# Kernel tuning notes

Measured on AMD Instinct MI355X. Metric: run time of the kernel, lower is better.

The kernel has to match this reference:

```python
import jax, jax.numpy as jnp
import numpy as np

B, S, D_IN, D, H, HD, HALF, L = 64, 500, 64, 128, 8, 16, 5, 2
WIN = 2 * HALF + 1  # 11 attended positions per query
EPS = 1e-12  # HF layer_norm_eps default


def _ln(x, g, b):
    m = x.mean(-1, keepdims=True)
    v = ((x - m) ** 2).mean(-1, keepdims=True)
    return (x - m) / jnp.sqrt(v + EPS) * g + b


def setup_inputs() -> dict:
    key = jax.random.key(0)
    ks = jax.random.split(key, 24)
    n = lambda i, shape: jax.random.normal(ks[i], shape, jnp.float32) * 0.02
    return {
        "x": jax.random.normal(ks[0], (B, S, D_IN), jnp.float32),
        "W_in": n(1, (D_IN, D)), "b_in": jnp.zeros((D,), jnp.float32),
        "pos_emb": n(2, (512, D)), "tt_emb": n(3, (D,)),
        "ln_emb_g": jnp.ones((D,), jnp.float32), "ln_emb_b": jnp.zeros((D,), jnp.float32),
        "Wq": n(4, (L, D, D)), "bq": jnp.zeros((L, D), jnp.float32),
        "Wk": n(5, (L, D, D)), "bk": jnp.zeros((L, D), jnp.float32),
        "Wv": n(6, (L, D, D)), "bv": jnp.zeros((L, D), jnp.float32),
        "Wo": n(7, (L, D, D)), "bo": jnp.zeros((L, D), jnp.float32),
        "ln1_g": jnp.ones((L, D), jnp.float32), "ln1_b": jnp.zeros((L, D), jnp.float32),
        "Wi": n(8, (L, D, 512)), "bi": jnp.zeros((L, 512), jnp.float32),
        "Wo2": n(9, (L, 512, D)), "bo2": jnp.zeros((L, D), jnp.float32),
        "ln2_g": jnp.ones((L, D), jnp.float32), "ln2_b": jnp.zeros((L, D), jnp.float32),
        "W_cls": n(10, (D, 2)), "b_cls": jnp.zeros((2,), jnp.float32),
    }


def reference(x, W_in, b_in, pos_emb, tt_emb, ln_emb_g, ln_emb_b,
              Wq, bq, Wk, bk, Wv, bv, Wo, bo, ln1_g, ln1_b,
              Wi, bi, Wo2, bo2, ln2_g, ln2_b, W_cls, b_cls):
    # input projection + RoBERTa-style embeddings (position ids start at padding_idx+1=2)
    h = x @ W_in + b_in
    pos_ids = 2 + jnp.arange(S)
    h = _ln(h + pos_emb[pos_ids] + tt_emb, ln_emb_g, ln_emb_b)

    # sliding-window gather indices: each query attends [i-HALF, i+HALF]
    idx = jnp.arange(S)[:, None] + jnp.arange(-HALF, HALF + 1)[None, :]
    valid = (idx >= 0) & (idx < S)
    idxc = jnp.clip(idx, 0, S - 1)
    scale = 1.0 / jnp.sqrt(jnp.float32(HD))

    for l in range(L):
        qh = (h @ Wq[l] + bq[l]).reshape(B, S, H, HD).transpose(0, 2, 1, 3)
        kh = (h @ Wk[l] + bk[l]).reshape(B, S, H, HD).transpose(0, 2, 1, 3)
        vh = (h @ Wv[l] + bv[l]).reshape(B, S, H, HD).transpose(0, 2, 1, 3)
        kk = kh[:, :, idxc]
        scores = jnp.einsum('bhsd,bhswd->bhsw', qh * scale, kk)
        scores = jnp.where(valid, scores, -jnp.inf)
        probs = jax.nn.softmax(scores, axis=-1)
        vv = vh[:, :, idxc]
        ctx = jnp.einsum('bhsw,bhswd->bhsd', probs, vv)
        ctx = ctx.transpose(0, 2, 1, 3).reshape(B, S, D)
        h = _ln(ctx @ Wo[l] + bo[l] + h, ln1_g[l], ln1_b[l])
        ff = jax.nn.gelu(h @ Wi[l] + bi[l], approximate=False) @ Wo2[l] + bo2[l]
        h = _ln(ff + h, ln2_g[l], ln2_b[l])

    pooled = h.mean(axis=1)  # mean over sequence
    return pooled @ W_cls + b_cls
```

## Files before the change

kernel.cpp:

```cpp
#include <hip/hip_runtime.h>
#include <hip/hip_bf16.h>
#include <math.h>

#define BB 64
#define SS 500
#define DIN 64
#define DD 128
#define HH 8
#define HDIM 16
#define HALF_ 5
#define WINW 11
#define LL 2
#define FF 512
#define MM (BB*SS)
#define LN_EPS 1e-12f

typedef __attribute__((ext_vector_type(8))) short short8;
typedef __attribute__((ext_vector_type(4))) float f32x4;

__global__ __launch_bounds__(256) void k_prep(
    const float* __restrict__ Wq, const float* __restrict__ Wk,
    const float* __restrict__ Wv, const float* __restrict__ Wo,
    const float* __restrict__ Wi, const float* __restrict__ Wo2,
    __hip_bfloat16* __restrict__ wT)
{
    const int m = blockIdx.y;
    const int l = m / 6, t = m % 6;
    const float* src; int Kd, Nd, kshift, doff;
    switch (t) {
      case 0:  src = Wq  + l*16384; Kd=128; Nd=128; kshift=7; doff=0;      break;
      case 1:  src = Wk  + l*16384; Kd=128; Nd=128; kshift=7; doff=16384;  break;
      case 2:  src = Wv  + l*16384; Kd=128; Nd=128; kshift=7; doff=32768;  break;
      case 3:  src = Wo  + l*16384; Kd=128; Nd=128; kshift=7; doff=49152;  break;
      case 4:  src = Wi  + l*65536; Kd=128; Nd=512; kshift=7; doff=65536;  break;
      default: src = Wo2 + l*65536; Kd=512; Nd=128; kshift=9; doff=131072; break;
    }
    __hip_bfloat16* dst = wT + l*196608 + doff;
    const int NK = Kd * Nd;
    int e = (blockIdx.x * 256 + threadIdx.x) * 4;
    if (e >= NK) return;
    #pragma unroll
    for (int j = 0; j < 4; ++j, ++e) {
        int n = e >> kshift, kx = e & (Kd - 1);
        dst[(size_t)n * Kd + kx] = __float2bfloat16(src[(size_t)kx * Nd + n]);
    }
}

__global__ __launch_bounds__(256) void k_embed(
    const float* __restrict__ x, const float* __restrict__ Win,
    const float* __restrict__ bin, const float* __restrict__ pos,
    const float* __restrict__ tt, const float* __restrict__ g,
    const float* __restrict__ be, float* __restrict__ h,
    __hip_bfloat16* __restrict__ hbf)
{
    __shared__ float WinS[DIN][DD];
    __shared__ float xs[16][DIN];
    __shared__ float rs[4][2];

    const int tid = threadIdx.x;
    const int d    = tid & 127;
    const int rp   = tid >> 7;
    const int wid  = tid >> 6;
    const int row0 = blockIdx.x * 16;

    #pragma unroll
    for (int it = 0; it < 8; ++it) {
        int lin = it * 1024 + tid * 4;
        *(float4*)&WinS[lin >> 7][lin & 127] = *(const float4*)(Win + lin);
    }
    {
        int lin = tid * 4;
        *(float4*)&xs[lin >> 6][lin & 63] =
            *(const float4*)(x + (size_t)row0 * DIN + lin);
    }
    __syncthreads();

    const float bd = bin[d] + tt[d];

    for (int it = 0; it < 8; ++it) {
        const int r   = it * 2 + rp;
        const int row = row0 + r;
        const int s   = row % SS;

        float acc = bd + pos[(size_t)(2 + s) * DD + d];
        #pragma unroll 8
        for (int i = 0; i < DIN; ++i) acc += xs[r][i] * WinS[i][d];

        float s1 = acc, s2 = acc * acc;
        #pragma unroll
        for (int off = 1; off < 64; off <<= 1) {
            s1 += __shfl_xor(s1, off);
            s2 += __shfl_xor(s2, off);
        }
        if ((tid & 63) == 0) { rs[wid][0] = s1; rs[wid][1] = s2; }
        __syncthreads();
        const float S1 = rs[rp * 2][0] + rs[rp * 2 + 1][0];
        const float S2 = rs[rp * 2][1] + rs[rp * 2 + 1][1];
        const float mean = S1 * (1.0f / DD);
        const float var  = S2 * (1.0f / DD) - mean * mean;
        const float rstd = rsqrtf(var + LN_EPS);
        const float o = (acc - mean) * rstd * g[d] + be[d];
        h[(size_t)row * DD + d]   = o;
        hbf[(size_t)row * DD + d] = __float2bfloat16(o);
        __syncthreads();
    }
}

#define GEMM_MAIN(Abf, lda, Kdim, WTbf, ldw, n0w)                             \
    __shared__ __align__(16) __hip_bfloat16 As[64][72];                       \
    __shared__ __align__(16) __hip_bfloat16 Ws[128][72];                      \
    const int tid = threadIdx.x;                                              \
    const int wid = tid >> 6;                                                 \
    const int l15 = tid & 15;                                                 \
    const int l4  = (tid & 63) >> 4;                                          \
    const int m0  = blockIdx.x * 64;                                          \
    f32x4 acc[8];                                                             \
    _Pragma("unroll")                                                         \
    for (int n = 0; n < 8; ++n) acc[n] = (f32x4){0.f, 0.f, 0.f, 0.f};         \
    for (int k0 = 0; k0 < (Kdim); k0 += 64) {                                 \
        _Pragma("unroll")                                                     \
        for (int it = 0; it < 2; ++it) {                                      \
            int lin = it * 2048 + tid * 8;                                    \
            int r = lin >> 6, c = lin & 63;                                   \
            *(uint4*)&As[r][c] =                                              \
                *(const uint4*)((Abf) + (size_t)(m0 + r) * (lda) + k0 + c);   \
        }                                                                     \
        _Pragma("unroll")                                                     \
        for (int it = 0; it < 4; ++it) {                                      \
            int lin = it * 2048 + tid * 8;                                    \
            int r = lin >> 6, c = lin & 63;                                   \
            *(uint4*)&Ws[r][c] =                                              \
                *(const uint4*)((WTbf) + (size_t)((n0w) + r) * (ldw) + k0 + c); \
        }                                                                     \
        __syncthreads();                                                      \
        _Pragma("unroll")                                                     \
        for (int kc = 0; kc < 64; kc += 32) {                                 \
            short8 a0 = *(const short8*)&As[wid * 16 + l15][kc + l4 * 8];     \
            _Pragma("unroll")                                                 \
            for (int n = 0; n < 8; ++n) {                                     \
                short8 bf = *(const short8*)&Ws[n * 16 + l15][kc + l4 * 8];   \
                acc[n] = __builtin_amdgcn_mfma_f32_16x16x32_bf16(a0, bf, acc[n], 0, 0, 0); \
            }                                                                 \
        }                                                                     \
        __syncthreads();                                                      \
    }

__global__ __launch_bounds__(256, 4) void k_gemm_qkv(
    const __hip_bfloat16* __restrict__ hbf,
    const __hip_bfloat16* __restrict__ wTq, const __hip_bfloat16* __restrict__ wTk,
    const __hip_bfloat16* __restrict__ wTv,
    const float* __restrict__ bq, const float* __restrict__ bk,
    const float* __restrict__ bv,
    __hip_bfloat16* __restrict__ q, __hip_bfloat16* __restrict__ k,
    __hip_bfloat16* __restrict__ v)
{
    const __hip_bfloat16* WT; const float* bias; __hip_bfloat16* out;
    if (blockIdx.y == 0)      { WT = wTq; bias = bq; out = q; }
    else if (blockIdx.y == 1) { WT = wTk; bias = bk; out = k; }
    else                      { WT = wTv; bias = bv; out = v; }
    GEMM_MAIN(hbf, DD, DD, WT, DD, 0)
    #pragma unroll
    for (int qq = 0; qq < 4; ++qq) {
        const int row = m0 + wid * 16 + l4 * 4 + qq;
        #pragma unroll
        for (int n = 0; n < 8; ++n) {
            const int col = n * 16 + l15;
            out[(size_t)row * DD + col] = __float2bfloat16(acc[n][qq] + bias[col]);
        }
    }
}

__global__ __launch_bounds__(256, 4) void k_gemm_gelu(
    const __hip_bfloat16* __restrict__ hbf,
    const __hip_bfloat16* __restrict__ wTi,
    const float* __restrict__ bias, __hip_bfloat16* __restrict__ hid)
{
    const int n0g = blockIdx.y * 128;
    GEMM_MAIN(hbf, DD, DD, wTi, DD, n0g)
    #pragma unroll
    for (int qq = 0; qq < 4; ++qq) {
        const int row = m0 + wid * 16 + l4 * 4 + qq;
        #pragma unroll
        for (int n = 0; n < 8; ++n) {
            const int col = n0g + n * 16 + l15;
            float val = acc[n][qq] + bias[col];
            val = 0.5f * val * (1.f + erff(val * 0.70710678118f));
            hid[(size_t)row * FF + col] = __float2bfloat16(val);
        }
    }
}

__global__ __launch_bounds__(256, 4) void k_gemm_lnres(
    const __hip_bfloat16* __restrict__ Abf, int lda, int Kdim,
    const __hip_bfloat16* __restrict__ WT,
    const float* __restrict__ bias, const float* __restrict__ res,
    const float* __restrict__ g, const float* __restrict__ bt,
    float* __restrict__ outF, __hip_bfloat16* __restrict__ outB)
{
    GEMM_MAIN(Abf, lda, Kdim, WT, Kdim, 0)
    #pragma unroll
    for (int qq = 0; qq < 4; ++qq) {
        const int row = m0 + wid * 16 + l4 * 4 + qq;
        float vals[8]; float s1 = 0.f, s2 = 0.f;
        #pragma unroll
        for (int n = 0; n < 8; ++n) {
            const int col = n * 16 + l15;
            float val = acc[n][qq] + bias[col] + res[(size_t)row * DD + col];
            vals[n] = val; s1 += val; s2 += val * val;
        }
        #pragma unroll
        for (int off = 1; off < 16; off <<= 1) {
            s1 += __shfl_xor(s1, off, 16);
            s2 += __shfl_xor(s2, off, 16);
        }
        const float mean = s1 * (1.0f / DD);
        const float var  = s2 * (1.0f / DD) - mean * mean;
        const float rstd = rsqrtf(var + LN_EPS);
        #pragma unroll
        for (int n = 0; n < 8; ++n) {
            const int col = n * 16 + l15;
            const float o = (vals[n] - mean) * rstd * g[col] + bt[col];
            outF[(size_t)row * DD + col] = o;
            outB[(size_t)row * DD + col] = __float2bfloat16(o);
        }
    }
}

__global__ __launch_bounds__(256) void k_attn(
    const __hip_bfloat16* __restrict__ q, const __hip_bfloat16* __restrict__ k,
    const __hip_bfloat16* __restrict__ v, __hip_bfloat16* __restrict__ ctx)
{
    __shared__ float kS[26][17], vS[26][17], qS[16][17], pS[16][16];

    const int tile = blockIdx.x, hh = blockIdx.y, b = blockIdx.z;
    const int s0  = tile * 16;
    const int tid = threadIdx.x;

    for (int e = tid; e < 26 * 16; e += 256) {
        const int r = e >> 4, d = e & 15;
        const int sr = s0 - 5 + r;
        const bool ok = (sr >= 0) && (sr < SS);
        const size_t src = ((size_t)(b * SS + (ok ? sr : 0))) * DD + hh * HDIM + d;
        kS[r][d] = ok ? __bfloat162float(k[src]) : 0.f;
        vS[r][d] = ok ? __bfloat162float(v[src]) : 0.f;
    }
    {
        const int gg = tid >> 4, d = tid & 15;
        const int sq = s0 + gg;
        qS[gg][d] = (sq < SS)
            ? __bfloat162float(q[((size_t)(b * SS + sq)) * DD + hh * HDIM + d]) : 0.f;
    }
    __syncthreads();

    const int g = tid >> 4;
    const int w = tid & 15;
    const int sq = s0 + g;
    const int sw = sq + w - HALF_;
    const bool valid = (w < WINW) && (sw >= 0) && (sw < SS) && (sq < SS);

    float sc = 0.f;
    #pragma unroll
    for (int d = 0; d < HDIM; ++d) sc += qS[g][d] * kS[g + w][d];
    sc = valid ? sc * 0.25f : -INFINITY;

    float mx = sc;
    #pragma unroll
    for (int off = 1; off < 16; off <<= 1) mx = fmaxf(mx, __shfl_xor(mx, off, 16));
    float p = valid ? __expf(sc - mx) : 0.f;
    float den = p;
    #pragma unroll
    for (int off = 1; off < 16; off <<= 1) den += __shfl_xor(den, off, 16);
    pS[g][w] = p / den;

    float cd = 0.f;
    #pragma unroll
    for (int w2 = 0; w2 < WINW; ++w2) cd += pS[g][w2] * vS[g + w2][w];
    if (sq < SS)
        ctx[((size_t)(b * SS + sq)) * DD + hh * HDIM + w] = __float2bfloat16(cd);
}

__global__ __launch_bounds__(128) void k_final(
    const float* __restrict__ h, const float* __restrict__ Wc,
    const float* __restrict__ bc, float* __restrict__ out)
{
    const int b = blockIdx.x, d = threadIdx.x;
    float p = 0.f;
    for (int s = 0; s < SS; ++s) p += h[((size_t)(b * SS + s)) * DD + d];
    p *= (1.0f / SS);
    float l0 = p * Wc[d * 2 + 0];
    float l1 = p * Wc[d * 2 + 1];
    #pragma unroll
    for (int off = 1; off < 64; off <<= 1) {
        l0 += __shfl_xor(l0, off);
        l1 += __shfl_xor(l1, off);
    }
    __shared__ float r[2][2];
    const int wid = d >> 6;
    if ((d & 63) == 0) { r[wid][0] = l0; r[wid][1] = l1; }
    __syncthreads();
    if (d == 0) {
        out[b * 2 + 0] = r[0][0] + r[1][0] + bc[0];
        out[b * 2 + 1] = r[0][1] + r[1][1] + bc[1];
    }
}

extern "C" void kernel_launch(void* const* d_in, const int* in_sizes, int n_in,
                              void* d_out, int out_size, void* d_ws, size_t ws_size,
                              hipStream_t stream)
{
    const float* x      = (const float*)d_in[0];
    const float* W_in   = (const float*)d_in[1];
    const float* b_in   = (const float*)d_in[2];
    const float* pos    = (const float*)d_in[3];
    const float* tt     = (const float*)d_in[4];
    const float* lng    = (const float*)d_in[5];
    const float* lnb    = (const float*)d_in[6];
    const float* Wq     = (const float*)d_in[7];
    const float* bq     = (const float*)d_in[8];
    const float* Wk     = (const float*)d_in[9];
    const float* bk     = (const float*)d_in[10];
    const float* Wv     = (const float*)d_in[11];
    const float* bv     = (const float*)d_in[12];
    const float* Wo     = (const float*)d_in[13];
    const float* bo     = (const float*)d_in[14];
    const float* ln1g   = (const float*)d_in[15];
    const float* ln1b   = (const float*)d_in[16];
    const float* Wi     = (const float*)d_in[17];
    const float* bi     = (const float*)d_in[18];
    const float* Wo2    = (const float*)d_in[19];
    const float* bo2    = (const float*)d_in[20];
    const float* ln2g   = (const float*)d_in[21];
    const float* ln2b   = (const float*)d_in[22];
    const float* Wc     = (const float*)d_in[23];
    const float* bc     = (const float*)d_in[24];

    float*          ws    = (float*)d_ws;
    float*          h     = ws;
    __hip_bfloat16* hbf   = (__hip_bfloat16*)(ws + 4096000);
    __hip_bfloat16* ctxbf = (__hip_bfloat16*)(ws + 6144000);
    __hip_bfloat16* wT    = (__hip_bfloat16*)(ws + 8192000);
    __hip_bfloat16* q     = (__hip_bfloat16*)(ws + 8400000);
    __hip_bfloat16* kk    = (__hip_bfloat16*)(ws + 10448000);
    __hip_bfloat16* vv    = (__hip_bfloat16*)(ws + 12496000);
    __hip_bfloat16* hid   = q;

    k_prep<<<dim3(64, 12), 256, 0, stream>>>(Wq, Wk, Wv, Wo, Wi, Wo2, wT);
    k_embed<<<MM / 16, 256, 0, stream>>>(x, W_in, b_in, pos, tt, lng, lnb, h, hbf);

    for (int l = 0; l < LL; ++l) {
        const __hip_bfloat16* wTq  = wT + l * 196608;
        const __hip_bfloat16* wTk  = wTq + 16384;
        const __hip_bfloat16* wTv  = wTq + 32768;
        const __hip_bfloat16* wTo  = wTq + 49152;
        const __hip_bfloat16* wTi  = wTq + 65536;
        const __hip_bfloat16* wTo2 = wTq + 131072;

        k_gemm_qkv<<<dim3(MM / 64, 3), 256, 0, stream>>>(
            hbf, wTq, wTk, wTv, bq + l * DD, bk + l * DD, bv + l * DD, q, kk, vv);

        k_attn<<<dim3(32, HH, BB), 256, 0, stream>>>(q, kk, vv, ctxbf);

        k_gemm_lnres<<<dim3(MM / 64, 1), 256, 0, stream>>>(
            ctxbf, DD, DD, wTo, bo + l * DD, h, ln1g + l * DD, ln1b + l * DD, h, hbf);

        k_gemm_gelu<<<dim3(MM / 64, 4), 256, 0, stream>>>(
            hbf, wTi, bi + l * FF, hid);

        k_gemm_lnres<<<dim3(MM / 64, 1), 256, 0, stream>>>(
            hid, FF, FF, wTo2, bo2 + l * DD, h, ln2g + l * DD, ln2b + l * DD, h, hbf);
    }

    k_final<<<BB, 128, 0, stream>>>(h, Wc, bc, (float*)d_out);
}
```

Before: 392.0 us.

## Fuse QKV projection, windowed attention, output projection and LayerNorm into one kernel

Replaces the separate QKV GEMM, attention and Wo+LN kernels with one fused kernel per 32-row sequence tile. It recomputes Q/K/V for a 42-row halo in shared memory, does the sliding-window softmax there and applies the output projection with residual LayerNorm, so the q/k/v/ctx tensors no longer go through global memory. The embedding input projection also becomes an MFMA bf16 GEMM, with a separate x-to-bf16 conversion kernel. The cost is redundant halo compute (10 extra rows per 32), weights read straight from global in the fused kernel, only 1024 blocks of work, and ping-pong h buffers.

```diff
diff --git a/kernel.cpp b/kernel.cpp
--- a/kernel.cpp
+++ b/kernel.cpp
@@ -22,20 +22,26 @@
     const float* __restrict__ Wq, const float* __restrict__ Wk,
     const float* __restrict__ Wv, const float* __restrict__ Wo,
     const float* __restrict__ Wi, const float* __restrict__ Wo2,
-    __hip_bfloat16* __restrict__ wT)
+    const float* __restrict__ Win, __hip_bfloat16* __restrict__ wT)
 {
     const int m = blockIdx.y;
-    const int l = m / 6, t = m % 6;
     const float* src; int Kd, Nd, kshift, doff;
-    switch (t) {
-      case 0:  src = Wq  + l*16384; Kd=128; Nd=128; kshift=7; doff=0;      break;
-      case 1:  src = Wk  + l*16384; Kd=128; Nd=128; kshift=7; doff=16384;  break;
-      case 2:  src = Wv  + l*16384; Kd=128; Nd=128; kshift=7; doff=32768;  break;
-      case 3:  src = Wo  + l*16384; Kd=128; Nd=128; kshift=7; doff=49152;  break;
-      case 4:  src = Wi  + l*65536; Kd=128; Nd=512; kshift=7; doff=65536;  break;
-      default: src = Wo2 + l*65536; Kd=512; Nd=128; kshift=9; doff=131072; break;
-    }
-    __hip_bfloat16* dst = wT + l*196608 + doff;
+    if (m == 12) {
+        src = Win; Kd = 64; Nd = 128; kshift = 6; doff = 393216;
+    } else {
+        const int l = m / 6, t = m % 6;
+        int toff;
+        switch (t) {
+          case 0:  src = Wq  + l*16384; Kd=128; Nd=128; kshift=7; toff=0;      break;
+          case 1:  src = Wk  + l*16384; Kd=128; Nd=128; kshift=7; toff=16384;  break;
+          case 2:  src = Wv  + l*16384; Kd=128; Nd=128; kshift=7; toff=32768;  break;
+          case 3:  src = Wo  + l*16384; Kd=128; Nd=128; kshift=7; toff=49152;  break;
+          case 4:  src = Wi  + l*65536; Kd=128; Nd=512; kshift=7; toff=65536;  break;
+          default: src = Wo2 + l*65536; Kd=512; Nd=128; kshift=9; toff=131072; break;
+        }
+        doff = l*196608 + toff;
+    }
+    __hip_bfloat16* dst = wT + doff;
     const int NK = Kd * Nd;
     int e = (blockIdx.x * 256 + threadIdx.x) * 4;
     if (e >= NK) return;
@@ -46,64 +52,18 @@
     }
 }
 
-__global__ __launch_bounds__(256) void k_embed(
-    const float* __restrict__ x, const float* __restrict__ Win,
-    const float* __restrict__ bin, const float* __restrict__ pos,
-    const float* __restrict__ tt, const float* __restrict__ g,
-    const float* __restrict__ be, float* __restrict__ h,
-    __hip_bfloat16* __restrict__ hbf)
-{
-    __shared__ float WinS[DIN][DD];
-    __shared__ float xs[16][DIN];
-    __shared__ float rs[4][2];
-
-    const int tid = threadIdx.x;
-    const int d    = tid & 127;
-    const int rp   = tid >> 7;
-    const int wid  = tid >> 6;
-    const int row0 = blockIdx.x * 16;
-
-    #pragma unroll
-    for (int it = 0; it < 8; ++it) {
-        int lin = it * 1024 + tid * 4;
-        *(float4*)&WinS[lin >> 7][lin & 127] = *(const float4*)(Win + lin);
-    }
-    {
-        int lin = tid * 4;
-        *(float4*)&xs[lin >> 6][lin & 63] =
-            *(const float4*)(x + (size_t)row0 * DIN + lin);
-    }
-    __syncthreads();
-
-    const float bd = bin[d] + tt[d];
-
-    for (int it = 0; it < 8; ++it) {
-        const int r   = it * 2 + rp;
-        const int row = row0 + r;
-        const int s   = row % SS;
-
-        float acc = bd + pos[(size_t)(2 + s) * DD + d];
-        #pragma unroll 8
-        for (int i = 0; i < DIN; ++i) acc += xs[r][i] * WinS[i][d];
-
-        float s1 = acc, s2 = acc * acc;
-        #pragma unroll
-        for (int off = 1; off < 64; off <<= 1) {
-            s1 += __shfl_xor(s1, off);
-            s2 += __shfl_xor(s2, off);
-        }
-        if ((tid & 63) == 0) { rs[wid][0] = s1; rs[wid][1] = s2; }
-        __syncthreads();
-        const float S1 = rs[rp * 2][0] + rs[rp * 2 + 1][0];
-        const float S2 = rs[rp * 2][1] + rs[rp * 2 + 1][1];
-        const float mean = S1 * (1.0f / DD);
-        const float var  = S2 * (1.0f / DD) - mean * mean;
-        const float rstd = rsqrtf(var + LN_EPS);
-        const float o = (acc - mean) * rstd * g[d] + be[d];
-        h[(size_t)row * DD + d]   = o;
-        hbf[(size_t)row * DD + d] = __float2bfloat16(o);
-        __syncthreads();
-    }
+__global__ __launch_bounds__(256) void k_xcvt(
+    const float* __restrict__ x, __hip_bfloat16* __restrict__ xbf)
+{
+    int i = (blockIdx.x * 256 + threadIdx.x) * 4;
+    if (i >= MM * DIN) return;
+    float4 v = *(const float4*)(x + i);
+    ushort4 o;
+    __hip_bfloat16 t0 = __float2bfloat16(v.x); o.x = *(unsigned short*)&t0;
+    __hip_bfloat16 t1 = __float2bfloat16(v.y); o.y = *(unsigned short*)&t1;
+    __hip_bfloat16 t2 = __float2bfloat16(v.z); o.z = *(unsigned short*)&t2;
+    __hip_bfloat16 t3 = __float2bfloat16(v.w); o.w = *(unsigned short*)&t3;
+    *(ushort4*)(xbf + i) = o;
 }
 
 #define GEMM_MAIN(Abf, lda, Kdim, WTbf, ldw, n0w)                             \
@@ -145,27 +105,205 @@
         __syncthreads();                                                      \
     }
 
-__global__ __launch_bounds__(256, 4) void k_gemm_qkv(
-    const __hip_bfloat16* __restrict__ hbf,
-    const __hip_bfloat16* __restrict__ wTq, const __hip_bfloat16* __restrict__ wTk,
-    const __hip_bfloat16* __restrict__ wTv,
-    const float* __restrict__ bq, const float* __restrict__ bk,
-    const float* __restrict__ bv,
-    __hip_bfloat16* __restrict__ q, __hip_bfloat16* __restrict__ k,
-    __hip_bfloat16* __restrict__ v)
-{
-    const __hip_bfloat16* WT; const float* bias; __hip_bfloat16* out;
-    if (blockIdx.y == 0)      { WT = wTq; bias = bq; out = q; }
-    else if (blockIdx.y == 1) { WT = wTk; bias = bk; out = k; }
-    else                      { WT = wTv; bias = bv; out = v; }
-    GEMM_MAIN(hbf, DD, DD, WT, DD, 0)
+__global__ __launch_bounds__(256, 4) void k_embed(
+    const __hip_bfloat16* __restrict__ xbf, const __hip_bfloat16* __restrict__ wInT,
+    const float* __restrict__ bin, const float* __restrict__ pos,
+    const float* __restrict__ tt, const float* __restrict__ g,
+    const float* __restrict__ be, float* __restrict__ h,
+    __hip_bfloat16* __restrict__ hbf)
+{
+    GEMM_MAIN(xbf, DIN, DIN, wInT, DIN, 0)
     #pragma unroll
     for (int qq = 0; qq < 4; ++qq) {
         const int row = m0 + wid * 16 + l4 * 4 + qq;
+        const int s = row % SS;
+        float vals[8]; float s1 = 0.f, s2 = 0.f;
         #pragma unroll
         for (int n = 0; n < 8; ++n) {
             const int col = n * 16 + l15;
-            out[(size_t)row * DD + col] = __float2bfloat16(acc[n][qq] + bias[col]);
+            float val = acc[n][qq] + bin[col] + tt[col] + pos[(size_t)(2 + s) * DD + col];
+            vals[n] = val; s1 += val; s2 += val * val;
+        }
+        #pragma unroll
+        for (int o = 1; o < 16; o <<= 1) {
+            s1 += __shfl_xor(s1, o, 16);
+            s2 += __shfl_xor(s2, o, 16);
+        }
+        const float mean = s1 * (1.0f / DD);
+        const float var  = s2 * (1.0f / DD) - mean * mean;
+        const float rstd = rsqrtf(var + LN_EPS);
+        #pragma unroll
+        for (int n = 0; n < 8; ++n) {
+            const int col = n * 16 + l15;
+            const float o = (vals[n] - mean) * rstd * g[col] + be[col];
+            h[(size_t)row * DD + col]   = o;
+            hbf[(size_t)row * DD + col] = __float2bfloat16(o);
+        }
+    }
+}
+
+__global__ __launch_bounds__(256) void k_fused(
+    const __hip_bfloat16* __restrict__ hin,
+    const __hip_bfloat16* __restrict__ wTq, const __hip_bfloat16* __restrict__ wTk,
+    const __hip_bfloat16* __restrict__ wTv, const __hip_bfloat16* __restrict__ wTo,
+    const float* __restrict__ bq, const float* __restrict__ bk,
+    const float* __restrict__ bv, const float* __restrict__ bo,
+    const float* __restrict__ hres,
+    const float* __restrict__ g1, const float* __restrict__ bt1,
+    float* __restrict__ hout, __hip_bfloat16* __restrict__ hbfout)
+{
+    __shared__ __align__(16) char smem[49472];
+    __hip_bfloat16* kS   = (__hip_bfloat16*)smem;
+    __hip_bfloat16* vS   = (__hip_bfloat16*)(smem + 13056);
+    __hip_bfloat16* hS   = (__hip_bfloat16*)(smem + 26112);
+    __hip_bfloat16* qS   = (__hip_bfloat16*)(smem + 39168);
+    float*          pS   = (float*)(smem + 47872);
+    float*          rsum = (float*)(smem + 48960);
+    __hip_bfloat16* ctxS = hS;
+
+    const int tid = threadIdx.x;
+    const int wid = tid >> 6, l15 = tid & 15, l4 = (tid & 63) >> 4;
+    const int b = blockIdx.y;
+    const int s0 = blockIdx.x * 32;
+
+    #pragma unroll
+    for (int it = 0; it < 3; ++it) {
+        int lin = it * 256 + tid;
+        int r = lin >> 4, c8 = (lin & 15) * 8;
+        int s = s0 - 5 + r;
+        uint4 val = {0, 0, 0, 0};
+        if (s >= 0 && s < SS)
+            val = *(const uint4*)(hin + ((size_t)(b * SS + s)) * DD + c8);
+        *(uint4*)&hS[r * 136 + c8] = val;
+    }
+    __syncthreads();
+
+    for (int j = wid; j < 9; j += 4) {
+        const int out = j / 3, rt = j % 3;
+        const __hip_bfloat16* WT = (out == 0) ? wTq : ((out == 1) ? wTk : wTv);
+        const float* bias = (out == 0) ? bq : ((out == 1) ? bk : bv);
+        for (int n = 0; n < 8; ++n) {
+            f32x4 a = (f32x4){0.f, 0.f, 0.f, 0.f};
+            #pragma unroll
+            for (int kc = 0; kc < 4; ++kc) {
+                short8 af  = *(const short8*)&hS[(rt * 16 + l15) * 136 + kc * 32 + l4 * 8];
+                short8 bfg = *(const short8*)(WT + (size_t)(n * 16 + l15) * DD + kc * 32 + l4 * 8);
+                a = __builtin_amdgcn_mfma_f32_16x16x32_bf16(af, bfg, a, 0, 0, 0);
+            }
+            const int col = n * 16 + l15;
+            const float bcol = bias[col];
+            #pragma unroll
+            for (int qq = 0; qq < 4; ++qq) {
+                const int row = rt * 16 + l4 * 4 + qq;
+                const float val = a[qq] + bcol;
+                if (out == 0) {
+                    if (row >= 5 && row < 37)
+                        qS[(row - 5) * 136 + col] = __float2bfloat16(val * 0.25f);
+                } else if (out == 1) {
+                    kS[row * 136 + col] = __float2bfloat16(val);
+                } else {
+                    vS[row * 136 + col] = __float2bfloat16(val);
+                }
+            }
+        }
+    }
+    __syncthreads();
+
+    {
+        const int g = tid >> 4, wl = tid & 15;
+        for (int qh = 0; qh < 2; ++qh) {
+            const int qrow = qh * 16 + g;
+            const int sq = s0 + qrow;
+            const int sk = sq + wl - HALF_;
+            const bool valid = (wl < WINW) && (sq < SS) && (sk >= 0) && (sk < SS);
+            #pragma unroll
+            for (int hh = 0; hh < 8; ++hh) {
+                const int off = hh * 16;
+                float sc = 0.f;
+                const unsigned* qp = (const unsigned*)&qS[qrow * 136 + off];
+                const unsigned* kp = (const unsigned*)&kS[(qrow + wl) * 136 + off];
+                #pragma unroll
+                for (int d2 = 0; d2 < 8; ++d2) {
+                    unsigned qu = qp[d2], ku = kp[d2];
+                    sc += __uint_as_float(qu << 16) * __uint_as_float(ku << 16)
+                        + __uint_as_float(qu & 0xffff0000u) * __uint_as_float(ku & 0xffff0000u);
+                }
+                sc = valid ? sc : -INFINITY;
+                float mx = sc;
+                #pragma unroll
+                for (int o = 1; o < 16; o <<= 1) mx = fmaxf(mx, __shfl_xor(mx, o, 16));
+                float p = valid ? __expf(sc - mx) : 0.f;
+                float den = p;
+                #pragma unroll
+                for (int o = 1; o < 16; o <<= 1) den += __shfl_xor(den, o, 16);
+                const float inv = (den > 0.f) ? 1.f / den : 0.f;
+                pS[g * 17 + wl] = p;
+                float cd = 0.f;
+                #pragma unroll
+                for (int w2 = 0; w2 < WINW; ++w2)
+                    cd += pS[g * 17 + w2] * __bfloat162float(vS[(qrow + w2) * 136 + off + wl]);
+                ctxS[qrow * 136 + off + wl] = __float2bfloat16(cd * inv);
+            }
+        }
+    }
+    __syncthreads();
+
+    const int rt2 = wid & 1, nh = wid >> 1;
+    f32x4 ac[4];
+    #pragma unroll
+    for (int n4 = 0; n4 < 4; ++n4) {
+        ac[n4] = (f32x4){0.f, 0.f, 0.f, 0.f};
+        const int n = nh * 4 + n4;
+        #pragma unroll
+        for (int kc = 0; kc < 4; ++kc) {
+            short8 af  = *(const short8*)&ctxS[(rt2 * 16 + l15) * 136 + kc * 32 + l4 * 8];
+            short8 bfg = *(const short8*)(wTo + (size_t)(n * 16 + l15) * DD + kc * 32 + l4 * 8);
+            ac[n4] = __builtin_amdgcn_mfma_f32_16x16x32_bf16(af, bfg, ac[n4], 0, 0, 0);
+        }
+    }
+    float vals[4][4];
+    #pragma unroll
+    for (int qq = 0; qq < 4; ++qq) {
+        const int r16 = l4 * 4 + qq;
+        const int qrow = rt2 * 16 + r16;
+        const int sq = s0 + qrow;
+        const bool vr = (sq < SS);
+        float s1 = 0.f, s2 = 0.f;
+        #pragma unroll
+        for (int n4 = 0; n4 < 4; ++n4) {
+            const int col = (nh * 4 + n4) * 16 + l15;
+            const float resv = vr ? hres[((size_t)(b * SS + sq)) * DD + col] : 0.f;
+            const float val = ac[n4][qq] + bo[col] + resv;
+            vals[qq][n4] = val; s1 += val; s2 += val * val;
+        }
+        #pragma unroll
+        for (int o = 1; o < 16; o <<= 1) {
+            s1 += __shfl_xor(s1, o, 16);
+            s2 += __shfl_xor(s2, o, 16);
+        }
+        if (l15 == 0) {
+            rsum[rt2 * 64 + nh * 32 + r16 * 2]     = s1;
+            rsum[rt2 * 64 + nh * 32 + r16 * 2 + 1] = s2;
+        }
+    }
+    __syncthreads();
+    #pragma unroll
+    for (int qq = 0; qq < 4; ++qq) {
+        const int r16 = l4 * 4 + qq;
+        const int qrow = rt2 * 16 + r16;
+        const int sq = s0 + qrow;
+        if (sq >= SS) continue;
+        const float S1 = rsum[rt2 * 64 + r16 * 2]     + rsum[rt2 * 64 + 32 + r16 * 2];
+        const float S2 = rsum[rt2 * 64 + r16 * 2 + 1] + rsum[rt2 * 64 + 32 + r16 * 2 + 1];
+        const float mean = S1 * (1.0f / DD);
+        const float var  = S2 * (1.0f / DD) - mean * mean;
+        const float rstd = rsqrtf(var + LN_EPS);
+        #pragma unroll
+        for (int n4 = 0; n4 < 4; ++n4) {
+            const int col = (nh * 4 + n4) * 16 + l15;
+            const float o = (vals[qq][n4] - mean) * rstd * g1[col] + bt1[col];
+            hout[((size_t)(b * SS + sq)) * DD + col]   = o;
+            hbfout[((size_t)(b * SS + sq)) * DD + col] = __float2bfloat16(o);
         }
     }
 }
@@ -209,9 +347,9 @@
             vals[n] = val; s1 += val; s2 += val * val;
         }
         #pragma unroll
-        for (int off = 1; off < 16; off <<= 1) {
-            s1 += __shfl_xor(s1, off, 16);
-            s2 += __shfl_xor(s2, off, 16);
+        for (int o = 1; o < 16; o <<= 1) {
+            s1 += __shfl_xor(s1, o, 16);
+            s2 += __shfl_xor(s2, o, 16);
         }
         const float mean = s1 * (1.0f / DD);
         const float var  = s2 * (1.0f / DD) - mean * mean;
@@ -224,59 +362,6 @@
             outB[(size_t)row * DD + col] = __float2bfloat16(o);
         }
     }
-}
-
-__global__ __launch_bounds__(256) void k_attn(
-    const __hip_bfloat16* __restrict__ q, const __hip_bfloat16* __restrict__ k,
-    const __hip_bfloat16* __restrict__ v, __hip_bfloat16* __restrict__ ctx)
-{
-    __shared__ float kS[26][17], vS[26][17], qS[16][17], pS[16][16];
-
-    const int tile = blockIdx.x, hh = blockIdx.y, b = blockIdx.z;
-    const int s0  = tile * 16;
-    const int tid = threadIdx.x;
-
-    for (int e = tid; e < 26 * 16; e += 256) {
-        const int r = e >> 4, d = e & 15;
-        const int sr = s0 - 5 + r;
-        const bool ok = (sr >= 0) && (sr < SS);
-        const size_t src = ((size_t)(b * SS + (ok ? sr : 0))) * DD + hh * HDIM + d;
-        kS[r][d] = ok ? __bfloat162float(k[src]) : 0.f;
-        vS[r][d] = ok ? __bfloat162float(v[src]) : 0.f;
-    }
-    {
-        const int gg = tid >> 4, d = tid & 15;
-        const int sq = s0 + gg;
-        qS[gg][d] = (sq < SS)
-            ? __bfloat162float(q[((size_t)(b * SS + sq)) * DD + hh * HDIM + d]) : 0.f;
-    }
-    __syncthreads();
-
-    const int g = tid >> 4;
-    const int w = tid & 15;
-    const int sq = s0 + g;
-    const int sw = sq + w - HALF_;
-    const bool valid = (w < WINW) && (sw >= 0) && (sw < SS) && (sq < SS);
-
-    float sc = 0.f;
-    #pragma unroll
-    for (int d = 0; d < HDIM; ++d) sc += qS[g][d] * kS[g + w][d];
-    sc = valid ? sc * 0.25f : -INFINITY;
-
-    float mx = sc;
-    #pragma unroll
-    for (int off = 1; off < 16; off <<= 1) mx = fmaxf(mx, __shfl_xor(mx, off, 16));
-    float p = valid ? __expf(sc - mx) : 0.f;
-    float den = p;
-    #pragma unroll
-    for (int off = 1; off < 16; off <<= 1) den += __shfl_xor(den, off, 16);
-    pS[g][w] = p / den;
-
-    float cd = 0.f;
-    #pragma unroll
-    for (int w2 = 0; w2 < WINW; ++w2) cd += pS[g][w2] * vS[g + w2][w];
-    if (sq < SS)
-        ctx[((size_t)(b * SS + sq)) * DD + hh * HDIM + w] = __float2bfloat16(cd);
 }
 
 __global__ __launch_bounds__(128) void k_final(
@@ -334,19 +419,22 @@
     const float* Wc     = (const float*)d_in[23];
     const float* bc     = (const float*)d_in[24];
 
-    float*          ws    = (float*)d_ws;
-    float*          h     = ws;
-    __hip_bfloat16* hbf   = (__hip_bfloat16*)(ws + 4096000);
-    __hip_bfloat16* ctxbf = (__hip_bfloat16*)(ws + 6144000);
-    __hip_bfloat16* wT    = (__hip_bfloat16*)(ws + 8192000);
-    __hip_bfloat16* q     = (__hip_bfloat16*)(ws + 8400000);
-    __hip_bfloat16* kk    = (__hip_bfloat16*)(ws + 10448000);
-    __hip_bfloat16* vv    = (__hip_bfloat16*)(ws + 12496000);
-    __hip_bfloat16* hid   = q;
-
-    k_prep<<<dim3(64, 12), 256, 0, stream>>>(Wq, Wk, Wv, Wo, Wi, Wo2, wT);
-    k_embed<<<MM / 16, 256, 0, stream>>>(x, W_in, b_in, pos, tt, lng, lnb, h, hbf);
-
+    float*          ws   = (float*)d_ws;
+    float*          hA   = ws;
+    __hip_bfloat16* hbA  = (__hip_bfloat16*)(ws + 4096000);
+    __hip_bfloat16* xbf  = (__hip_bfloat16*)(ws + 6144000);
+    __hip_bfloat16* wT   = (__hip_bfloat16*)(ws + 7168000);
+    __hip_bfloat16* hid  = (__hip_bfloat16*)(ws + 7368704);
+    float*          hB   = ws + 15560704;
+    __hip_bfloat16* hbB  = (__hip_bfloat16*)(ws + 19656704);
+
+    k_prep<<<dim3(64, 13), 256, 0, stream>>>(Wq, Wk, Wv, Wo, Wi, Wo2, W_in, wT);
+    k_xcvt<<<2000, 256, 0, stream>>>(x, xbf);
+    k_embed<<<MM / 64, 256, 0, stream>>>(xbf, wT + 393216, b_in, pos, tt, lng, lnb,
+                                         hA, hbA);
+
+    float* hI = hA; __hip_bfloat16* hbI = hbA;
+    float* hO = hB; __hip_bfloat16* hbO = hbB;
     for (int l = 0; l < LL; ++l) {
         const __hip_bfloat16* wTq  = wT + l * 196608;
         const __hip_bfloat16* wTk  = wTq + 16384;
@@ -355,20 +443,21 @@
         const __hip_bfloat16* wTi  = wTq + 65536;
         const __hip_bfloat16* wTo2 = wTq + 131072;
 
-        k_gemm_qkv<<<dim3(MM / 64, 3), 256, 0, stream>>>(
-            hbf, wTq, wTk, wTv, bq + l * DD, bk + l * DD, bv + l * DD, q, kk, vv);
-
-        k_attn<<<dim3(32, HH, BB), 256, 0, stream>>>(q, kk, vv, ctxbf);
+        k_fused<<<dim3(16, BB), 256, 0, stream>>>(
+            hbI, wTq, wTk, wTv, wTo,
+            bq + l * DD, bk + l * DD, bv + l * DD, bo + l * DD,
+            hI, ln1g + l * DD, ln1b + l * DD, hO, hbO);
+
+        k_gemm_gelu<<<dim3(MM / 64, 4), 256, 0, stream>>>(
+            hbO, wTi, bi + l * FF, hid);
 
         k_gemm_lnres<<<dim3(MM / 64, 1), 256, 0, stream>>>(
-            ctxbf, DD, DD, wTo, bo + l * DD, h, ln1g + l * DD, ln1b + l * DD, h, hbf);
-
-        k_gemm_gelu<<<dim3(MM / 64, 4), 256, 0, stream>>>(
-            hbf, wTi, bi + l * FF, hid);
-
-        k_gemm_lnres<<<dim3(MM / 64, 1), 256, 0, stream>>>(
-            hid, FF, FF, wTo2, bo2 + l * DD, h, ln2g + l * DD, ln2b + l * DD, h, hbf);
-    }
-
-    k_final<<<BB, 128, 0, stream>>>(h, Wc, bc, (float*)d_out);
-}
+            hid, FF, FF, wTo2, bo2 + l * DD, hO, ln2g + l * DD, ln2b + l * DD,
+            hO, hbO);
+
+        float* tf = hI; hI = hO; hO = tf;
+        __hip_bfloat16* tb = hbI; hbI = hbO; hbO = tb;
+    }
+
+    k_final<<<BB, 128, 0, stream>>>(hI, Wc, bc, (float*)d_out);
+}
```

After: 394.0 us. No clear change (+0.5%).
